# Performance work log

Hardware: AMD Instinct MI355X
Metric: run time of the kernel (lower is better)

## Reference

```python
import jax, jax.numpy as jnp
import numpy as np

N = 100000
E = 1600000
IN_DIM = 128
HID_DIM = 128
OUT_DIM = 128


def _gcn_conv(x, W, b, row, col, n):
    # PyG GCNConv: x' = D^{-1/2} (A + I) D^{-1/2} (x W) + b, self-loops included
    xw = x @ W  # [n, dout]
    deg = jnp.zeros((n,), xw.dtype).at[col].add(1.0)  # in-degree incl self-loops
    dinv = jnp.where(deg > 0, jax.lax.rsqrt(deg), 0.0)
    norm = dinv[row] * dinv[col]  # [e]
    msg = xw[row] * norm[:, None]  # [e, dout] -- dominant memory traffic
    out = jax.ops.segment_sum(msg, col, num_segments=n)
    return out + b


def setup_inputs() -> dict:
    key = jax.random.key(0)
    k1, k2, k3, k4, k5, k6 = jax.random.split(key, 6)
    posts = jax.random.normal(k1, (N, IN_DIM), dtype=jnp.float32)
    edge_index = jax.random.randint(k2, (2, E), 0, N, dtype=jnp.int64)
    W1 = jax.random.normal(k3, (IN_DIM, HID_DIM), dtype=jnp.float32) * (1.0 / np.sqrt(IN_DIM))
    b1 = jnp.zeros((HID_DIM,), dtype=jnp.float32)
    W2 = jax.random.normal(k4, (HID_DIM + IN_DIM, OUT_DIM), dtype=jnp.float32) * (1.0 / np.sqrt(HID_DIM + IN_DIM))
    b2 = jnp.zeros((OUT_DIM,), dtype=jnp.float32)
    return {"posts": posts, "W1": W1, "b1": b1, "W2": W2, "b2": b2,
            "edge_index": edge_index, "rootIndex": 0}


def reference(posts, W1, b1, W2, b2, edge_index, rootIndex):
    n = posts.shape[0]
    loops = jnp.arange(n, dtype=edge_index.dtype)
    row = jnp.concatenate([edge_index[0], loops])
    col = jnp.concatenate([edge_index[1], loops])

    conv1_out = _gcn_conv(posts, W1, b1, row, col, n)  # [n, hid]
    post_root = jnp.broadcast_to(posts[rootIndex], (n, posts.shape[1]))
    conv1_root = jnp.broadcast_to(conv1_out[rootIndex], (n, conv1_out.shape[1]))

    conv2_in = jax.nn.relu(jnp.concatenate([conv1_out, post_root], axis=1))
    # dropout is identity at inference
    conv2_out = jax.nn.relu(_gcn_conv(conv2_in, W2, b2, row, col, n))

    feature = jnp.concatenate([conv1_root, conv2_out], axis=1)  # [n, hid+out]
    # avg_pool1d(kernel_size=3, stride=1) over the feature axis -> [n, hid+out-2]
    pooled = (feature[:, :-2] + feature[:, 1:-1] + feature[:, 2:]) * (1.0 / 3.0)
    return pooled
```

## Files before the change

kernel.cpp:

```cpp
#include <hip/hip_runtime.h>
#include <hip/hip_fp16.h>

#define DIM 128
#define CSTRIDE 64
typedef _Float16 half8 __attribute__((ext_vector_type(8)));
typedef float f32x4 __attribute__((ext_vector_type(4)));

__global__ void k_wprep(const float* __restrict__ W1, const float* __restrict__ W2,
                        __half* __restrict__ Wf1h, __half* __restrict__ Wf2h,
                        int* __restrict__ cnt, int N){
  const float* Wsrc = (blockIdx.x < 8) ? W1 : W2;
  _Float16* Wf = (_Float16*)((blockIdx.x < 8) ? Wf1h : Wf2h);
  int id   = (blockIdx.x & 7)*256 + threadIdx.x;
  int lane = id & 63;
  int ckc  = id >> 6;
  int kc   = ckc & 3, ct = ckc >> 2;
  int kbase = kc*32 + (lane >> 4)*8;
  int c     = ct*16 + (lane & 15);
  half8 v;
  #pragma unroll
  for (int i = 0; i < 8; i++)
    v[i] = (_Float16)Wsrc[(size_t)(kbase + i)*DIM + c];
  *(half8*)(Wf + (size_t)id*8) = v;
  for (int i = blockIdx.x*256 + threadIdx.x; i < N; i += 16*256)
    cnt[i] = 0;
}

template<int INH>
__device__ __forceinline__ void gemm_mfma(const void* __restrict__ Xv,
    const _Float16* __restrict__ Wf, const float* __restrict__ addvec,
    const int* __restrict__ cntp, __half* __restrict__ Yh, int N, int doRelu, int gb){
  int wid = threadIdx.x >> 6;
  int l   = threadIdx.x & 63;
  int g   = l >> 4;
  int lr  = l & 15;
  int rowA = gb*64 + wid*16 + lr;
  int rA   = (rowA < N) ? rowA : (N - 1);

  f32x4 acc[8];
  #pragma unroll
  for (int ct = 0; ct < 8; ct++) acc[ct] = (f32x4){0.f, 0.f, 0.f, 0.f};

  #pragma unroll
  for (int kc = 0; kc < 4; kc++){
    half8 a;
    if (INH){
      a = *(const half8*)((const _Float16*)Xv + (size_t)rA*DIM + kc*32 + g*8);
    } else {
      const float* xp = (const float*)Xv + (size_t)rA*DIM + kc*32 + g*8;
      float4 x0 = *(const float4*)xp;
      float4 x1 = *(const float4*)(xp + 4);
      a[0]=(_Float16)x0.x; a[1]=(_Float16)x0.y; a[2]=(_Float16)x0.z; a[3]=(_Float16)x0.w;
      a[4]=(_Float16)x1.x; a[5]=(_Float16)x1.y; a[6]=(_Float16)x1.z; a[7]=(_Float16)x1.w;
    }
    if (doRelu){
      #pragma unroll
      for (int i = 0; i < 8; i++) a[i] = (a[i] > (_Float16)0.f) ? a[i] : (_Float16)0.f;
    }
    #pragma unroll
    for (int ct = 0; ct < 8; ct++){
      half8 b = *(const half8*)(Wf + ((size_t)(ct*4 + kc)*64 + l)*8);
      acc[ct] = __builtin_amdgcn_mfma_f32_16x16x32_f16(a, b, acc[ct], 0, 0, 0);
    }
  }

  int m0 = gb*64 + wid*16 + g*4;
  float av[8];
  #pragma unroll
  for (int ct = 0; ct < 8; ct++) av[ct] = addvec ? addvec[ct*16 + lr] : 0.f;
  #pragma unroll
  for (int r = 0; r < 4; r++){
    int rr = m0 + r;
    if (rr < N){
      float dv = cntp ? rsqrtf((float)(cntp[rr] + 1)) : 1.f;
      #pragma unroll
      for (int ct = 0; ct < 8; ct++){
        float o = dv*(acc[ct][r] + av[ct]);
        Yh[(size_t)rr*DIM + ct*16 + lr] = __float2half(o);
      }
    }
  }
}

__global__ __launch_bounds__(256) void k_megaM(const float* __restrict__ posts,
    const __half* __restrict__ Wf1, __half* __restrict__ xw1u,
    const int* __restrict__ row, const int* __restrict__ col, int E,
    int* __restrict__ cnt, int* __restrict__ csrp, int N, int nG){
  int bid = blockIdx.x;
  int m = bid % 5;
  if (m == 0){
    int g = bid / 5;
    if (g < nG)
      gemm_mfma<0>(posts, (const _Float16*)Wf1, nullptr, nullptr, xw1u, N, 0, g);
  } else {
    int cb = (bid/5)*4 + (m - 1);
    int e = cb*256 + threadIdx.x;
    if (e < E){
      int c = col[e];
      int pos = atomicAdd(&cnt[c], 1);
      if (pos < CSTRIDE)
        csrp[(size_t)c*CSTRIDE + pos] = row[e];
    }
  }
}

__global__ __launch_bounds__(256) void k_megaC(const __half* __restrict__ c1h,
    const __half* __restrict__ Wf2, const float* __restrict__ cvec,
    const int* __restrict__ cnt, __half* __restrict__ xw2s,
    const float* __restrict__ cpool, float* __restrict__ outp, int N, int nG, int nF){
  int bid = blockIdx.x;
  if (bid < nG){
    gemm_mfma<1>(c1h, (const _Float16*)Wf2, cvec, cnt, xw2s, N, 1, bid);
  } else {
    int f = bid - nG;
    if (f >= nF) return;
    int total = N * 63;
    #pragma unroll
    for (int i = 0; i < 8; i++){
      int w = f*2048 + i*256 + threadIdx.x;
      if (w < total){
        unsigned int r  = (unsigned int)w / 63u;
        unsigned int c2 = (unsigned int)w - r*63u;
        float2 val = *(const float2*)(cpool + c2*2);
        *(float2*)(outp + (size_t)r*254 + c2*2) = val;
      }
    }
  }
}

__global__ void k_conv1(const __half* __restrict__ xw1u, const int* __restrict__ csrp,
                        const int* __restrict__ cnt,
                        const float* __restrict__ b, const int* __restrict__ rootIdx,
                        __half* __restrict__ outh, float* __restrict__ c1root, int N){
  int wid  = (blockIdx.x*blockDim.x + threadIdx.x) >> 6;
  if (wid >= N) return;
  int lane = threadIdx.x & 63;
  int half = lane >> 5;
  int sl   = lane & 31;
  int v = wid;
  float dv = rsqrtf((float)(cnt[v] + 1));
  long long o0 = (long long)v * CSTRIDE;
  int total = cnt[v] + 1;

  __half2 a01 = __float2half2_rn(0.f), a23 = __float2half2_rn(0.f);
  const __half* base = xw1u;

  auto idx = [&](int t){ return (t == 0) ? v : csrp[o0 + t - 1]; };
  auto dhv = [&](int r){ return __float2half_rn(rsqrtf((float)(cnt[r] + 1))); };
  auto accum = [&](uint2 wv, __half dh){
    __half2 d2 = __half2half2(dh);
    a01 = __hfma2(*(__half2*)&wv.x, d2, a01);
    a23 = __hfma2(*(__half2*)&wv.y, d2, a23);
  };

  int j = half;
  if (j + 14 < total){
    int nid[8];
    #pragma unroll
    for (int q = 0; q < 8; q++) nid[q] = idx(j + 2*q);
    while (j + 14 < total){
      int cur[8];
      #pragma unroll
      for (int q = 0; q < 8; q++) cur[q] = nid[q];
      int jn = j + 16;
      if (jn + 14 < total){
        #pragma unroll
        for (int q = 0; q < 8; q++) nid[q] = csrp[o0 + jn + 2*q - 1];
      }
      uint2 u[8]; __half dh[8];
      #pragma unroll
      for (int q = 0; q < 8; q++){
        u[q]  = *(const uint2*)(base + (size_t)cur[q]*DIM + sl*4);
        dh[q] = dhv(cur[q]);
      }
      #pragma unroll
      for (int q = 0; q < 8; q++) accum(u[q], dh[q]);
      j = jn;
    }
  }
  while (j + 6 < total){
    int i0 = idx(j), i1 = idx(j+2), i2 = idx(j+4), i3 = idx(j+6);
    uint2 u0 = *(const uint2*)(base + (size_t)i0*DIM + sl*4);
    uint2 u1 = *(const uint2*)(base + (size_t)i1*DIM + sl*4);
    uint2 u2 = *(const uint2*)(base + (size_t)i2*DIM + sl*4);
    uint2 u3 = *(const uint2*)(base + (size_t)i3*DIM + sl*4);
    __half d0 = dhv(i0), d1 = dhv(i1), d2 = dhv(i2), d3 = dhv(i3);
    accum(u0, d0); accum(u1, d1); accum(u2, d2); accum(u3, d3);
    j += 8;
  }
  for (; j < total; j += 2){
    int r = idx(j);
    uint2 u = *(const uint2*)(base + (size_t)r*DIM + sl*4);
    accum(u, dhv(r));
  }

  int r01 = __shfl_xor(*(int*)&a01, 32);
  int r23 = __shfl_xor(*(int*)&a23, 32);
  a01 = __hadd2(a01, *(__half2*)&r01);
  a23 = __hadd2(a23, *(__half2*)&r23);

  if (half == 0){
    float2 f01 = __half22float2(a01), f23 = __half22float2(a23);
    float4 bb = *(const float4*)(b + sl*4);
    float rx = dv*f01.x + bb.x, ry = dv*f01.y + bb.y;
    float rz = dv*f23.x + bb.z, rw = dv*f23.y + bb.w;
    __half2 h01 = __floats2half2_rn(rx, ry);
    __half2 h23 = __floats2half2_rn(rz, rw);
    uint2 u = make_uint2(*(unsigned int*)&h01, *(unsigned int*)&h23);
    *(uint2*)(outh + (size_t)v*DIM + sl*4) = u;
    if (v == rootIdx[0])
      *(float4*)(c1root + sl*4) = make_float4(rx, ry, rz, rw);
  }
}

__global__ void k_small(const float* __restrict__ posts, const float* __restrict__ W2,
                        const float* __restrict__ c1root, const int* __restrict__ rootIdx,
                        float* __restrict__ cvec, float* __restrict__ cpool){
  int j = threadIdx.x;
  int root = rootIdx[0];
  __shared__ float pr[DIM];
  __shared__ float cr[DIM];
  pr[j] = fmaxf(posts[(size_t)root*DIM + j], 0.f);
  cr[j] = c1root[j];
  __syncthreads();
  float s = 0.f;
  #pragma unroll 4
  for (int k = 0; k < DIM; k++) s += pr[k] * W2[(size_t)(DIM + k)*DIM + j];
  cvec[j] = s;
  cpool[j] = (j < 126) ? (cr[j] + cr[j+1] + cr[j+2]) * (1.f/3.f) : cr[j];
}

__global__ void k_conv2(const __half* __restrict__ xws, const int* __restrict__ csrp,
                        const int* __restrict__ cnt,
                        const float* __restrict__ b2,
                        const float* __restrict__ cpool, float* __restrict__ out, int N){
  int wid  = (blockIdx.x*blockDim.x + threadIdx.x) >> 6;
  if (wid >= N) return;
  int lane = threadIdx.x & 63;
  int half = lane >> 5;
  int sl   = lane & 31;
  int v = wid;
  float dv = rsqrtf((float)(cnt[v] + 1));
  long long o0 = (long long)v * CSTRIDE;
  int total = cnt[v] + 1;

  __half2 a01 = __float2half2_rn(0.f), a23 = __float2half2_rn(0.f);
  const __half* base = xws;

  auto idx = [&](int t){ return (t == 0) ? v : csrp[o0 + t - 1]; };
  auto accum = [&](uint2 wv){
    a01 = __hadd2(a01, *(__half2*)&wv.x);
    a23 = __hadd2(a23, *(__half2*)&wv.y);
  };

  int j = half;
  if (j + 14 < total){
    int nid[8];
    #pragma unroll
    for (int q = 0; q < 8; q++) nid[q] = idx(j + 2*q);
    while (j + 14 < total){
      int cur[8];
      #pragma unroll
      for (int q = 0; q < 8; q++) cur[q] = nid[q];
      int jn = j + 16;
      if (jn + 14 < total){
        #pragma unroll
        for (int q = 0; q < 8; q++) nid[q] = csrp[o0 + jn + 2*q - 1];
      }
      uint2 u[8];
      #pragma unroll
      for (int q = 0; q < 8; q++) u[q] = *(const uint2*)(base + (size_t)cur[q]*DIM + sl*4);
      #pragma unroll
      for (int q = 0; q < 8; q++) accum(u[q]);
      j = jn;
    }
  }
  while (j + 6 < total){
    int i0 = idx(j), i1 = idx(j+2), i2 = idx(j+4), i3 = idx(j+6);
    uint2 u0 = *(const uint2*)(base + (size_t)i0*DIM + sl*4);
    uint2 u1 = *(const uint2*)(base + (size_t)i1*DIM + sl*4);
    uint2 u2 = *(const uint2*)(base + (size_t)i2*DIM + sl*4);
    uint2 u3 = *(const uint2*)(base + (size_t)i3*DIM + sl*4);
    accum(u0); accum(u1); accum(u2); accum(u3);
    j += 8;
  }
  for (; j < total; j += 2){
    uint2 u = *(const uint2*)(base + (size_t)idx(j)*DIM + sl*4);
    accum(u);
  }

  int r01 = __shfl_xor(*(int*)&a01, 32);
  int r23 = __shfl_xor(*(int*)&a23, 32);
  a01 = __hadd2(a01, *(__half2*)&r01);
  a23 = __hadd2(a23, *(__half2*)&r23);

  if (half == 0){
    float2 f01 = __half22float2(a01), f23 = __half22float2(a23);
    float4 bb = *(const float4*)(b2 + sl*4);
    float o0v = fmaxf(dv*f01.x + bb.x, 0.f);
    float o1v = fmaxf(dv*f01.y + bb.y, 0.f);
    float o2v = fmaxf(dv*f23.x + bb.z, 0.f);
    float o3v = fmaxf(dv*f23.y + bb.w, 0.f);

    float pz = __shfl_up(o2v, 1);
    float pw = __shfl_up(o3v, 1);
    if (sl == 0){ pz = cpool[126]; pw = cpool[127]; }
    const float third = 1.f/3.f;
    float q0 = (pz + pw + o0v) * third;
    float q1 = (pw + o0v + o1v) * third;
    float q2 = (o0v + o1v + o2v) * third;
    float q3 = (o1v + o2v + o3v) * third;

    float* orow = out + (size_t)v*254;
    *(float2*)(orow + 126 + sl*4)     = make_float2(q0, q1);
    *(float2*)(orow + 126 + sl*4 + 2) = make_float2(q2, q3);
  }
}

extern "C" void kernel_launch(void* const* d_in, const int* in_sizes, int n_in,
                              void* d_out, int out_size, void* d_ws, size_t ws_size,
                              hipStream_t stream){
  const float* posts = (const float*)d_in[0];
  const float* W1    = (const float*)d_in[1];
  const float* b1    = (const float*)d_in[2];
  const float* W2    = (const float*)d_in[3];
  const float* b2    = (const float*)d_in[4];
  const int*   eidx  = (const int*)d_in[5];
  const int*   rootI = (const int*)d_in[6];
  int N = in_sizes[0] / DIM;
  int E = in_sizes[5] / 2;
  const int* row = eidx;
  const int* col = eidx + E;

  char* p = (char*)d_ws;
  auto alloc = [&](size_t bytes)->void*{
    void* q = (void*)p; p += (bytes + 255) & ~(size_t)255; return q;
  };
  __half* xw1u  = (__half*)alloc((size_t)N*DIM*2);
  __half* xw2s  = (__half*)alloc((size_t)N*DIM*2);
  __half* c1h   = (__half*)alloc((size_t)N*DIM*2);
  __half* Wf1   = (__half*)alloc((size_t)DIM*DIM*2);
  __half* Wf2   = (__half*)alloc((size_t)DIM*DIM*2);
  float* c1root = (float*)alloc(DIM*4);
  float* cvec   = (float*)alloc(DIM*4);
  float* cpool  = (float*)alloc(DIM*4);
  int*   cnt    = (int*)alloc((size_t)N*4);
  int*   csrp   = (int*)alloc((size_t)N*CSTRIDE*4);

  int nG = (N + 63) / 64;
  int nC = (E + 255) / 256;
  int q5 = (nG > (nC + 3)/4) ? nG : (nC + 3)/4;
  int nF = (N*63 + 2047) / 2048;

  k_wprep<<<16, 256, 0, stream>>>(W1, W2, Wf1, Wf2, cnt, N);
  k_megaM<<<5*q5, 256, 0, stream>>>(posts, Wf1, xw1u, row, col, E, cnt, csrp, N, nG);
  k_conv1<<<(N + 3)/4, 256, 0, stream>>>(xw1u, csrp, cnt, b1, rootI, c1h, c1root, N);
  k_small<<<1, 128, 0, stream>>>(posts, W2, c1root, rootI, cvec, cpool);
  k_megaC<<<nG + nF, 256, 0, stream>>>(c1h, Wf2, cvec, cnt, xw2s, cpool,
                                       (float*)d_out, N, nG, nF);
  k_conv2<<<(N + 3)/4, 256, 0, stream>>>(xw2s, csrp, cnt, b2, cpool,
                                         (float*)d_out, N);
}
```

Measured before the change: 267.4 us.

## Build CSR via two-pass bucketed counting sort instead of global atomics

Replaces direct per-edge global atomicAdd on per-node counters with a two-pass scheme. Edges are first binned into 512-node buckets, using shared-memory histograms and one global atomic per bucket per block. A new k_build kernel then ranks edges within each bucket using shared-memory atomics and writes the padded CSR plus the counts. This is meant to cut contended random global atomics and scattered writes, at the cost of an extra kernel, an intermediate pair buffer, and a per-bucket capacity cap (MAXBE) that could drop edges if a bucket overflows.

Result: faster. 241.0 us (median of 2 runs) (-9.9%).

```diff
diff --git a/kernel.cpp b/kernel.cpp
--- a/kernel.cpp
+++ b/kernel.cpp
@@ -3,12 +3,14 @@
 
 #define DIM 128
 #define CSTRIDE 64
+#define BSHIFT 9
+#define MAXBE 9216
 typedef _Float16 half8 __attribute__((ext_vector_type(8)));
 typedef float f32x4 __attribute__((ext_vector_type(4)));
 
 __global__ void k_wprep(const float* __restrict__ W1, const float* __restrict__ W2,
                         __half* __restrict__ Wf1h, __half* __restrict__ Wf2h,
-                        int* __restrict__ cnt, int N){
+                        int* __restrict__ bucketCur){
   const float* Wsrc = (blockIdx.x < 8) ? W1 : W2;
   _Float16* Wf = (_Float16*)((blockIdx.x < 8) ? Wf1h : Wf2h);
   int id   = (blockIdx.x & 7)*256 + threadIdx.x;
@@ -22,8 +24,7 @@
   for (int i = 0; i < 8; i++)
     v[i] = (_Float16)Wsrc[(size_t)(kbase + i)*DIM + c];
   *(half8*)(Wf + (size_t)id*8) = v;
-  for (int i = blockIdx.x*256 + threadIdx.x; i < N; i += 16*256)
-    cnt[i] = 0;
+  if (blockIdx.x == 0) bucketCur[threadIdx.x] = 0;
 }
 
 template<int INH>
@@ -82,26 +83,73 @@
   }
 }
 
-__global__ __launch_bounds__(256) void k_megaM(const float* __restrict__ posts,
+__global__ __launch_bounds__(256) void k_megaB(const float* __restrict__ posts,
     const __half* __restrict__ Wf1, __half* __restrict__ xw1u,
     const int* __restrict__ row, const int* __restrict__ col, int E,
-    int* __restrict__ cnt, int* __restrict__ csrp, int N, int nG){
+    int* __restrict__ bucketCur, uint2* __restrict__ spair, int N, int nG, int nCB){
+  __shared__ int hist[256];
+  __shared__ int sbase[256];
   int bid = blockIdx.x;
-  int m = bid % 5;
-  if (m == 0){
-    int g = bid / 5;
+  int m = bid % 3;
+  if (m < 2){
+    int g = (bid/3)*2 + m;
     if (g < nG)
       gemm_mfma<0>(posts, (const _Float16*)Wf1, nullptr, nullptr, xw1u, N, 0, g);
   } else {
-    int cb = (bid/5)*4 + (m - 1);
-    int e = cb*256 + threadIdx.x;
-    if (e < E){
-      int c = col[e];
-      int pos = atomicAdd(&cnt[c], 1);
-      if (pos < CSTRIDE)
-        csrp[(size_t)c*CSTRIDE + pos] = row[e];
-    }
-  }
+    int cb = bid / 3;
+    if (cb >= nCB) return;
+    int t = threadIdx.x;
+    hist[t] = 0;
+    __syncthreads();
+    int base_e = cb*2048 + t;
+    int bq[8], lr[8], rq[8], cq[8];
+    #pragma unroll
+    for (int q = 0; q < 8; q++){
+      int e = base_e + q*256;
+      if (e < E){
+        cq[q] = col[e];
+        rq[q] = row[e];
+        bq[q] = cq[q] >> BSHIFT;
+        lr[q] = atomicAdd(&hist[bq[q]], 1);
+      } else bq[q] = -1;
+    }
+    __syncthreads();
+    int h = hist[t];
+    if (h > 0) sbase[t] = atomicAdd(&bucketCur[t], h);
+    __syncthreads();
+    #pragma unroll
+    for (int q = 0; q < 8; q++){
+      if (bq[q] >= 0){
+        int p = sbase[bq[q]] + lr[q];
+        if (p < MAXBE)
+          spair[(size_t)bq[q]*MAXBE + p] = make_uint2((unsigned)rq[q], (unsigned)cq[q]);
+      }
+    }
+  }
+}
+
+__global__ __launch_bounds__(256) void k_build(const uint2* __restrict__ spair,
+    const int* __restrict__ bucketCur, int* __restrict__ csrp,
+    int* __restrict__ cnt, int N){
+  __shared__ int c512[512];
+  int b = blockIdx.x;
+  int t = threadIdx.x;
+  c512[t] = 0; c512[t + 256] = 0;
+  __syncthreads();
+  int nb = bucketCur[b]; if (nb > MAXBE) nb = MAXBE;
+  const uint2* sp = spair + (size_t)b*MAXBE;
+  for (int i = t; i < nb; i += 256){
+    uint2 pr = sp[i];
+    int c = (int)pr.y;
+    int rank = atomicAdd(&c512[c & 511], 1);
+    if (rank < CSTRIDE)
+      csrp[(size_t)c*CSTRIDE + rank] = (int)pr.x;
+  }
+  __syncthreads();
+  int n0 = (b << BSHIFT) + t;
+  if (n0 < N) cnt[n0] = c512[t];
+  int n1 = n0 + 256;
+  if (n1 < ((b + 1) << BSHIFT) && n1 < N) cnt[n1] = c512[t + 256];
 }
 
 __global__ __launch_bounds__(256) void k_megaC(const __half* __restrict__ c1h,
@@ -346,14 +394,18 @@
   float* cpool  = (float*)alloc(DIM*4);
   int*   cnt    = (int*)alloc((size_t)N*4);
   int*   csrp   = (int*)alloc((size_t)N*CSTRIDE*4);
-
-  int nG = (N + 63) / 64;
-  int nC = (E + 255) / 256;
-  int q5 = (nG > (nC + 3)/4) ? nG : (nC + 3)/4;
-  int nF = (N*63 + 2047) / 2048;
-
-  k_wprep<<<16, 256, 0, stream>>>(W1, W2, Wf1, Wf2, cnt, N);
-  k_megaM<<<5*q5, 256, 0, stream>>>(posts, Wf1, xw1u, row, col, E, cnt, csrp, N, nG);
+  int*   bCur   = (int*)alloc(256*4);
+  int    NBUCK  = (N + (1 << BSHIFT) - 1) >> BSHIFT;
+  uint2* spair  = (uint2*)alloc((size_t)NBUCK*MAXBE*8);
+
+  int nG  = (N + 63) / 64;
+  int nCB = (E + 2047) / 2048;
+  int q3  = ((nG + 1)/2 > nCB) ? (nG + 1)/2 : nCB;
+  int nF  = (N*63 + 2047) / 2048;
+
+  k_wprep<<<16, 256, 0, stream>>>(W1, W2, Wf1, Wf2, bCur);
+  k_megaB<<<3*q3, 256, 0, stream>>>(posts, Wf1, xw1u, row, col, E, bCur, spair, N, nG, nCB);
+  k_build<<<NBUCK, 256, 0, stream>>>(spair, bCur, csrp, cnt, N);
   k_conv1<<<(N + 3)/4, 256, 0, stream>>>(xw1u, csrp, cnt, b1, rootI, c1h, c1root, N);
   k_small<<<1, 128, 0, stream>>>(posts, W2, c1root, rootI, cvec, cpool);
   k_megaC<<<nG + nF, 256, 0, stream>>>(c1h, Wf2, cvec, cnt, xw2s, cpool,
```
